# Performance work log

Measured on AMD Instinct MI355X. Metric: run time of the kernel, lower is better.

## Reference

```python
import jax, jax.numpy as jnp
import numpy as np

B, S, E, D = 8, 2048, 1024, 64

def setup_inputs() -> dict:
    key = jax.random.key(0)
    k1, k2, k3, k4 = jax.random.split(key, 4)
    x = jax.random.normal(k1, (B, S, E), dtype=jnp.float32)
    attention_mask = jnp.ones((B, S, S), dtype=jnp.int32)
    scale = 1.0 / np.sqrt(E)
    Wq = jax.random.normal(k2, (E, D), dtype=jnp.float32) * scale
    Wk = jax.random.normal(k3, (E, D), dtype=jnp.float32) * scale
    Wv = jax.random.normal(k4, (E, D), dtype=jnp.float32) * scale
    return {"x": x, "attention_mask": attention_mask, "Wq": Wq, "Wk": Wk, "Wv": Wv}

def reference(x, attention_mask, Wq, Wk, Wv):
    # Q,K,V projections: [B,S,E] @ [E,D] -> [B,S,D]
    Q = jnp.einsum('bse,ed->bsd', x, Wq)
    K = jnp.einsum('bse,ed->bsd', x, Wk)
    V = jnp.einsum('bse,ed->bsd', x, Wv)
    d_head = Q.shape[-1]
    # scores: [B,S,S], scaled by sqrt(dim_head)
    scores = jnp.einsum('bqd,bkd->bqk', Q, K) / jnp.sqrt(jnp.asarray(d_head, Q.dtype))
    scores = jnp.where(attention_mask == 0, jnp.asarray(-jnp.inf, scores.dtype), scores)
    attn = jax.nn.softmax(scores, axis=-1)
    # dropout p=0.0 (eval mode) -> identity
    out = jnp.einsum('bqk,bkd->bqd', attn, V)
    return out
```

## Files before the change

kernel.cpp:

```cpp
#include <hip/hip_runtime.h>
#include <hip/hip_bf16.h>
#include <math.h>


typedef __attribute__((ext_vector_type(8))) short short8;
typedef __attribute__((ext_vector_type(4))) float v4f;

__device__ __forceinline__ unsigned short f2bf(float f) {
  unsigned int u = __float_as_uint(f);
  unsigned int r = (u + 0x7fffu + ((u >> 16) & 1u)) >> 16;
  return (unsigned short)r;
}

__global__ __launch_bounds__(256) void prep_wf(const float* __restrict__ Wq,
                                               const float* __restrict__ Wk,
                                               const float* __restrict__ Wv,
                                               unsigned short* __restrict__ Wf) {
  int t = blockIdx.x * 256 + threadIdx.x;
  int e0 = t * 4;
  int m = e0 >> 16;
  int rem = e0 & 65535;
  int k = rem >> 6, n0 = rem & 63;
  const float* W = (m == 0) ? Wq : (m == 1 ? Wk : Wv);
  float4 f4 = *reinterpret_cast<const float4*>(W + rem);
  int kt = k >> 6, rr = k & 63;
  int kk = rr >> 5, quad = (rr >> 3) & 3, j = k & 7;
  int cbase = kt * 24 + kk;
  float f[4] = {f4.x, f4.y, f4.z, f4.w};
#pragma unroll
  for (int c = 0; c < 4; c++) {
    int N = m * 64 + n0 + c;
    int nt = N >> 4, q = N & 15;
    int o = (((cbase + nt * 2) << 6) | (quad * 16 + q)) * 8 + j;
    Wf[o] = f2bf(f[c]);
  }
}

__global__ __launch_bounds__(512) void proj_kernel(const float* __restrict__ x,
                                                   const unsigned short* __restrict__ Wf,
                                                   unsigned short* __restrict__ Qg,
                                                   unsigned short* __restrict__ Kf,
                                                   unsigned short* __restrict__ Vf) {
  const int tid = threadIdx.x;
  const int w = tid >> 6;
  const int lane = tid & 63;
  const int q = lane & 15, quad = lane >> 4;
  const int rg = w >> 2, ng = w & 3;
  const int m0 = blockIdx.x * 32 + rg * 16;

  const float* xrow = x + (size_t)(m0 + q) * 1024 + quad * 8;
  const unsigned short* Wl = Wf + lane * 8;

  v4f acc[3];
#pragma unroll
  for (int i = 0; i < 3; i++) acc[i] = (v4f)(0.0f);

  float4 acur[4], anext[4];
  auto loadA = [&](int kt, float4 a[4]) {
    const float* p = xrow + kt * 64;
    a[0] = *reinterpret_cast<const float4*>(p);
    a[1] = *reinterpret_cast<const float4*>(p + 4);
    a[2] = *reinterpret_cast<const float4*>(p + 32);
    a[3] = *reinterpret_cast<const float4*>(p + 36);
  };

  short8 bcur[6], bnext[6];
  auto loadB = [&](int kt, short8 bb[6]) {
#pragma unroll
    for (int i = 0; i < 3; i++) {
      const size_t toff = ((size_t)kt * 24 + (ng * 3 + i) * 2) * 512;
      bb[2 * i + 0] = *reinterpret_cast<const short8*>(Wl + toff);
      bb[2 * i + 1] = *reinterpret_cast<const short8*>(Wl + toff + 512);
    }
  };

  loadA(0, acur);
  loadB(0, bcur);

  for (int kt = 0; kt < 16; kt++) {
    if (kt < 15) {
      loadA(kt + 1, anext);
      loadB(kt + 1, bnext);
    }
    short8 af0, af1;
    {
      float* f = reinterpret_cast<float*>(acur);
#pragma unroll
      for (int j = 0; j < 4; j++) { af0[j] = (short)f2bf(f[j]); af0[4 + j] = (short)f2bf(f[4 + j]); }
#pragma unroll
      for (int j = 0; j < 4; j++) { af1[j] = (short)f2bf(f[8 + j]); af1[4 + j] = (short)f2bf(f[12 + j]); }
    }
    __builtin_amdgcn_s_setprio(1);
#pragma unroll
    for (int i = 0; i < 3; i++) {
      acc[i] = __builtin_amdgcn_mfma_f32_16x16x32_bf16(af0, bcur[2 * i + 0], acc[i], 0, 0, 0);
      acc[i] = __builtin_amdgcn_mfma_f32_16x16x32_bf16(af1, bcur[2 * i + 1], acc[i], 0, 0, 0);
    }
    __builtin_amdgcn_s_setprio(0);
#pragma unroll
    for (int i = 0; i < 4; i++) acur[i] = anext[i];
#pragma unroll
    for (int i = 0; i < 6; i++) bcur[i] = bnext[i];
  }

#pragma unroll
  for (int i = 0; i < 3; i++) {
    const int n = (ng * 3 + i) * 16 + q;
#pragma unroll
    for (int r = 0; r < 4; r++) {
      const int m = m0 + quad * 4 + r;
      const unsigned short hv = f2bf(acc[i][r]);
      if (n < 64) {
        Qg[(size_t)m * 64 + n] = hv;
      } else if (n < 128) {
        const int d = n - 64, s = m;
        const int b = s >> 11, srem = s & 2047, g = srem >> 4, qi = srem & 15;
        const int kk2 = d >> 5, quad2 = (d >> 3) & 3, j2 = d & 7;
        Kf[((((size_t)b * 128 + g) * 2 + kk2) * 64 + quad2 * 16 + qi) * 8 + j2] = hv;
      } else {
        const int d = n - 128, s = m;
        const int b = s >> 11, srem = s & 2047, kt2 = srem >> 6, s6 = srem & 63;
        const int kk2 = s6 >> 5, quad2 = (s6 >> 3) & 3, j2 = s6 & 7;
        const int dt = d >> 4, qi = d & 15;
        Vf[(((((size_t)b * 32 + kt2) * 4 + dt) * 2 + kk2) * 64 + quad2 * 16 + qi) * 8 + j2] = hv;
      }
    }
  }
}

__global__ __launch_bounds__(256, 3) void attn_kernel(const unsigned short* __restrict__ Qg,
                                                      const unsigned short* __restrict__ Kf,
                                                      const unsigned short* __restrict__ Vf,
                                                      const int* __restrict__ maskg,
                                                      float* __restrict__ outg) {
  __shared__ __align__(16) unsigned short Pl[4][16][72];

  const int tid = threadIdx.x;
  const int bid = blockIdx.x;
  const int b = bid & 7, qt = bid >> 3;
  const int q0 = qt * 16;
  const int w = tid >> 6, lane = tid & 63;
  const int q = lane & 15, quad = lane >> 4;

  const size_t qbase = ((size_t)b * 2048 + q0 + q) * 64 + quad * 8;
  const short8 qf0 = *reinterpret_cast<const short8*>(&Qg[qbase]);
  const short8 qf1 = *reinterpret_cast<const short8*>(&Qg[qbase + 32]);

  short8 onesf;
#pragma unroll
  for (int j = 0; j < 8; j++) onesf[j] = (short)0x3F80;

  const unsigned short* Kb = Kf + (size_t)b * 131072 + lane * 8;
  const unsigned short* Vb = Vf + (size_t)b * 131072 + lane * 8;
  const int* mb = maskg + ((size_t)b * 2048 + q0 + quad) * 2048 + q * 4;

  v4f o_acc[4], l_acc;
#pragma unroll
  for (int dt = 0; dt < 4; dt++) o_acc[dt] = (v4f)(0.0f);
  l_acc = (v4f)(0.0f);

  const float SC = 0.125f * 1.4426950408889634f;
  const int kt0 = w * 8;

  auto loadK = [&](int kt, short8 kk[8]) {
#pragma unroll
    for (int f = 0; f < 8; f++)
      kk[f] = *reinterpret_cast<const short8*>(Kb + ((size_t)kt * 8 + f) * 512);
  };

  unsigned zb = 0;
  {
    int4 m4[4];
#pragma unroll
    for (int j = 0; j < 4; j++)
      m4[j] = *reinterpret_cast<const int4*>(mb + (size_t)j * 8192 + kt0 * 64);
#pragma unroll
    for (int j = 0; j < 4; j++)
      zb |= ((unsigned)(m4[j].x == 0) << (j * 4)) | ((unsigned)(m4[j].y == 0) << (j * 4 + 1)) |
            ((unsigned)(m4[j].z == 0) << (j * 4 + 2)) | ((unsigned)(m4[j].w == 0) << (j * 4 + 3));
  }

  short8 kcur[8], knext[8];
  loadK(kt0, kcur);

#pragma unroll
  for (int it = 0; it < 8; it++) {
    const int kt = kt0 + it;

    int4 m4[4];
    if (it < 7) {
#pragma unroll
      for (int j = 0; j < 4; j++)
        m4[j] = *reinterpret_cast<const int4*>(mb + (size_t)j * 8192 + (kt + 1) * 64);
    }

    v4f s_acc[4];
    __builtin_amdgcn_s_setprio(1);
#pragma unroll
    for (int nt = 0; nt < 4; nt++) {
      s_acc[nt] = __builtin_amdgcn_mfma_f32_16x16x32_bf16(qf0, kcur[nt * 2 + 0], (v4f)(0.0f), 0, 0, 0);
      s_acc[nt] = __builtin_amdgcn_mfma_f32_16x16x32_bf16(qf1, kcur[nt * 2 + 1], s_acc[nt], 0, 0, 0);
    }
    __builtin_amdgcn_s_setprio(0);

    if (it < 7) loadK(kt + 1, knext);

    short8 vf[8];
#pragma unroll
    for (int f = 0; f < 8; f++)
      vf[f] = *reinterpret_cast<const short8*>(Vb + ((size_t)kt * 8 + f) * 512);

#pragma unroll
    for (int nt = 0; nt < 4; nt++)
#pragma unroll
      for (int r = 0; r < 4; r++)
        Pl[w][quad * 4 + r][nt * 16 + q] = f2bf(exp2f(s_acc[nt][r] * SC));

    if (__any(zb != 0u)) {
#pragma unroll
      for (int j = 0; j < 4; j++)
#pragma unroll
        for (int c = 0; c < 4; c++)
          if ((zb >> (j * 4 + c)) & 1u) Pl[w][j * 4 + quad][q * 4 + c] = 0;
    }

    const short8 pf0 = *reinterpret_cast<const short8*>(&Pl[w][q][quad * 8]);
    const short8 pf1 = *reinterpret_cast<const short8*>(&Pl[w][q][32 + quad * 8]);

    __builtin_amdgcn_s_setprio(1);
#pragma unroll
    for (int dt = 0; dt < 4; dt++) {
      o_acc[dt] = __builtin_amdgcn_mfma_f32_16x16x32_bf16(pf0, vf[dt * 2 + 0], o_acc[dt], 0, 0, 0);
      o_acc[dt] = __builtin_amdgcn_mfma_f32_16x16x32_bf16(pf1, vf[dt * 2 + 1], o_acc[dt], 0, 0, 0);
    }
    l_acc = __builtin_amdgcn_mfma_f32_16x16x32_bf16(pf0, onesf, l_acc, 0, 0, 0);
    l_acc = __builtin_amdgcn_mfma_f32_16x16x32_bf16(pf1, onesf, l_acc, 0, 0, 0);
    __builtin_amdgcn_s_setprio(0);

    if (it < 7) {
#pragma unroll
      for (int f = 0; f < 8; f++) kcur[f] = knext[f];
      zb = 0;
#pragma unroll
      for (int j = 0; j < 4; j++)
        zb |= ((unsigned)(m4[j].x == 0) << (j * 4)) | ((unsigned)(m4[j].y == 0) << (j * 4 + 1)) |
              ((unsigned)(m4[j].z == 0) << (j * 4 + 2)) | ((unsigned)(m4[j].w == 0) << (j * 4 + 3));
    }
  }

  __syncthreads();
  float* Osf = reinterpret_cast<float*>(&Pl[0][0][0]);
  float* Lsf = Osf + 2 * 16 * 68;

  if (w >= 2) {
    const int wi = w - 2;
#pragma unroll
    for (int r = 0; r < 4; r++) {
      const int row = quad * 4 + r;
#pragma unroll
      for (int dt = 0; dt < 4; dt++) Osf[(wi * 16 + row) * 68 + dt * 16 + q] = o_acc[dt][r];
      if (q == 0) Lsf[wi * 16 + row] = l_acc[r];
    }
  }
  __syncthreads();
  if (w < 2) {
#pragma unroll
    for (int r = 0; r < 4; r++) {
      const int row = quad * 4 + r;
#pragma unroll
      for (int dt = 0; dt < 4; dt++) o_acc[dt][r] += Osf[(w * 16 + row) * 68 + dt * 16 + q];
      l_acc[r] += Lsf[w * 16 + row];
    }
  }
  __syncthreads();
  if (w == 1) {
#pragma unroll
    for (int r = 0; r < 4; r++) {
      const int row = quad * 4 + r;
#pragma unroll
      for (int dt = 0; dt < 4; dt++) Osf[row * 68 + dt * 16 + q] = o_acc[dt][r];
      if (q == 0) Lsf[row] = l_acc[r];
    }
  }
  __syncthreads();
  if (w == 0) {
#pragma unroll
    for (int r = 0; r < 4; r++) {
      const int row = quad * 4 + r;
      const float inv = 1.0f / (l_acc[r] + Lsf[row]);
      const size_t orow = ((size_t)b * 2048 + q0 + row) * 64;
#pragma unroll
      for (int dt = 0; dt < 4; dt++)
        outg[orow + dt * 16 + q] = (o_acc[dt][r] + Osf[row * 68 + dt * 16 + q]) * inv;
    }
  }
}

extern "C" void kernel_launch(void* const* d_in, const int* in_sizes, int n_in,
                              void* d_out, int out_size, void* d_ws, size_t ws_size,
                              hipStream_t stream) {
  const float* x = (const float*)d_in[0];
  const int* mask = (const int*)d_in[1];
  const float* Wq = (const float*)d_in[2];
  const float* Wk = (const float*)d_in[3];
  const float* Wv = (const float*)d_in[4];
  float* out = (float*)d_out;

  char* ws = (char*)d_ws;
  unsigned short* Qg = (unsigned short*)(ws);
  unsigned short* Kf = (unsigned short*)(ws + (size_t)(2 << 20));
  unsigned short* Vf = (unsigned short*)(ws + (size_t)(4 << 20));
  unsigned short* Wf = (unsigned short*)(ws + (size_t)(6 << 20));

  prep_wf<<<192, 256, 0, stream>>>(Wq, Wk, Wv, Wf);
  proj_kernel<<<512, 512, 0, stream>>>(x, Wf, Qg, Kf, Vf);
  attn_kernel<<<1024, 256, 0, stream>>>(Qg, Kf, Vf, mask, out);
}
```

Before: 295.0 us.

## Precompute mask bitmasks in prep kernel and drop register double-buffers

Mask reading and compression into 16-bit zero-bitmasks moves from the attention kernel into a widened prep kernel, which also still converts the weights. The attention kernel then reads compact bitmasks instead of int32 mask tiles in its inner loop. Separately, the K and B operand prefetches now write into the current buffers after the MFMAs rather than into separate next buffers, and proj_kernel gets an occupancy hint, all to reduce register pressure. The mask must still be read in full by the prep kernel, and the reused buffers can serialise loads behind compute.

```diff
diff --git a/kernel.cpp b/kernel.cpp
--- a/kernel.cpp
+++ b/kernel.cpp
@@ -12,35 +12,52 @@
   return (unsigned short)r;
 }
 
-__global__ __launch_bounds__(256) void prep_wf(const float* __restrict__ Wq,
-                                               const float* __restrict__ Wk,
-                                               const float* __restrict__ Wv,
-                                               unsigned short* __restrict__ Wf) {
-  int t = blockIdx.x * 256 + threadIdx.x;
-  int e0 = t * 4;
-  int m = e0 >> 16;
-  int rem = e0 & 65535;
-  int k = rem >> 6, n0 = rem & 63;
-  const float* W = (m == 0) ? Wq : (m == 1 ? Wk : Wv);
-  float4 f4 = *reinterpret_cast<const float4*>(W + rem);
-  int kt = k >> 6, rr = k & 63;
-  int kk = rr >> 5, quad = (rr >> 3) & 3, j = k & 7;
-  int cbase = kt * 24 + kk;
-  float f[4] = {f4.x, f4.y, f4.z, f4.w};
-#pragma unroll
-  for (int c = 0; c < 4; c++) {
-    int N = m * 64 + n0 + c;
-    int nt = N >> 4, q = N & 15;
-    int o = (((cbase + nt * 2) << 6) | (quad * 16 + q)) * 8 + j;
-    Wf[o] = f2bf(f[c]);
-  }
-}
-
-__global__ __launch_bounds__(512) void proj_kernel(const float* __restrict__ x,
-                                                   const unsigned short* __restrict__ Wf,
-                                                   unsigned short* __restrict__ Qg,
-                                                   unsigned short* __restrict__ Kf,
-                                                   unsigned short* __restrict__ Vf) {
+__global__ __launch_bounds__(256) void prep_kernel(const float* __restrict__ Wq,
+                                                   const float* __restrict__ Wk,
+                                                   const float* __restrict__ Wv,
+                                                   const int* __restrict__ maskg,
+                                                   unsigned short* __restrict__ Wf,
+                                                   unsigned short* __restrict__ zbg) {
+  const int t = blockIdx.x * 256 + threadIdx.x;
+  const int lane = t & 63, kt = (t >> 6) & 31, qt = (t >> 11) & 127, b = t >> 18;
+  const int q = lane & 15, quad = lane >> 4;
+  const int* mp = maskg + ((size_t)(b * 2048 + qt * 16 + quad)) * 2048 + kt * 64 + q * 4;
+  unsigned zb = 0;
+#pragma unroll
+  for (int j = 0; j < 4; j++) {
+    int4 m4 = *reinterpret_cast<const int4*>(mp + (size_t)j * 8192);
+    zb |= ((unsigned)(m4.x == 0) << (j * 4)) | ((unsigned)(m4.y == 0) << (j * 4 + 1)) |
+          ((unsigned)(m4.z == 0) << (j * 4 + 2)) | ((unsigned)(m4.w == 0) << (j * 4 + 3));
+  }
+  zbg[t] = (unsigned short)zb;
+
+  const bool doW = (t < 49152);
+  if (doW) {
+    int e0 = t * 4;
+    int m = e0 >> 16;
+    int rem = e0 & 65535;
+    int k = rem >> 6, n0 = rem & 63;
+    const float* W = (m == 0) ? Wq : (m == 1 ? Wk : Wv);
+    float4 f4 = *reinterpret_cast<const float4*>(W + rem);
+    int kt2 = k >> 6, rr = k & 63;
+    int kk = rr >> 5, quad2 = (rr >> 3) & 3, j = k & 7;
+    int cbase = kt2 * 24 + kk;
+    float f[4] = {f4.x, f4.y, f4.z, f4.w};
+#pragma unroll
+    for (int c = 0; c < 4; c++) {
+      int N = m * 64 + n0 + c;
+      int nt = N >> 4, qq = N & 15;
+      int o = (((cbase + nt * 2) << 6) | (quad2 * 16 + qq)) * 8 + j;
+      Wf[o] = f2bf(f[c]);
+    }
+  }
+}
+
+__global__ __launch_bounds__(512, 4) void proj_kernel(const float* __restrict__ x,
+                                                      const unsigned short* __restrict__ Wf,
+                                                      unsigned short* __restrict__ Qg,
+                                                      unsigned short* __restrict__ Kf,
+                                                      unsigned short* __restrict__ Vf) {
   const int tid = threadIdx.x;
   const int w = tid >> 6;
   const int lane = tid & 63;
@@ -64,7 +81,7 @@
     a[3] = *reinterpret_cast<const float4*>(p + 36);
   };
 
-  short8 bcur[6], bnext[6];
+  short8 bcur[6];
   auto loadB = [&](int kt, short8 bb[6]) {
 #pragma unroll
     for (int i = 0; i < 3; i++) {
@@ -78,10 +95,7 @@
   loadB(0, bcur);
 
   for (int kt = 0; kt < 16; kt++) {
-    if (kt < 15) {
-      loadA(kt + 1, anext);
-      loadB(kt + 1, bnext);
-    }
+    if (kt < 15) loadA(kt + 1, anext);
     short8 af0, af1;
     {
       float* f = reinterpret_cast<float*>(acur);
@@ -97,10 +111,9 @@
       acc[i] = __builtin_amdgcn_mfma_f32_16x16x32_bf16(af1, bcur[2 * i + 1], acc[i], 0, 0, 0);
     }
     __builtin_amdgcn_s_setprio(0);
+    if (kt < 15) loadB(kt + 1, bcur);
 #pragma unroll
     for (int i = 0; i < 4; i++) acur[i] = anext[i];
-#pragma unroll
-    for (int i = 0; i < 6; i++) bcur[i] = bnext[i];
   }
 
 #pragma unroll
@@ -131,7 +144,7 @@
 __global__ __launch_bounds__(256, 3) void attn_kernel(const unsigned short* __restrict__ Qg,
                                                       const unsigned short* __restrict__ Kf,
                                                       const unsigned short* __restrict__ Vf,
-                                                      const int* __restrict__ maskg,
+                                                      const unsigned short* __restrict__ zbg,
                                                       float* __restrict__ outg) {
   __shared__ __align__(16) unsigned short Pl[4][16][72];
 
@@ -152,7 +165,6 @@
 
   const unsigned short* Kb = Kf + (size_t)b * 131072 + lane * 8;
   const unsigned short* Vb = Vf + (size_t)b * 131072 + lane * 8;
-  const int* mb = maskg + ((size_t)b * 2048 + q0 + quad) * 2048 + q * 4;
 
   v4f o_acc[4], l_acc;
 #pragma unroll
@@ -161,6 +173,13 @@
 
   const float SC = 0.125f * 1.4426950408889634f;
   const int kt0 = w * 8;
+
+  unsigned short zbs[8];
+  {
+    const unsigned short* zbp = zbg + (((size_t)b * 128 + qt) * 32 + kt0) * 64 + lane;
+#pragma unroll
+    for (int it = 0; it < 8; it++) zbs[it] = zbp[it * 64];
+  }
 
   auto loadK = [&](int kt, short8 kk[8]) {
 #pragma unroll
@@ -168,31 +187,12 @@
       kk[f] = *reinterpret_cast<const short8*>(Kb + ((size_t)kt * 8 + f) * 512);
   };
 
-  unsigned zb = 0;
-  {
-    int4 m4[4];
-#pragma unroll
-    for (int j = 0; j < 4; j++)
-      m4[j] = *reinterpret_cast<const int4*>(mb + (size_t)j * 8192 + kt0 * 64);
-#pragma unroll
-    for (int j = 0; j < 4; j++)
-      zb |= ((unsigned)(m4[j].x == 0) << (j * 4)) | ((unsigned)(m4[j].y == 0) << (j * 4 + 1)) |
-            ((unsigned)(m4[j].z == 0) << (j * 4 + 2)) | ((unsigned)(m4[j].w == 0) << (j * 4 + 3));
-  }
-
-  short8 kcur[8], knext[8];
+  short8 kcur[8];
   loadK(kt0, kcur);
 
 #pragma unroll
   for (int it = 0; it < 8; it++) {
     const int kt = kt0 + it;
-
-    int4 m4[4];
-    if (it < 7) {
-#pragma unroll
-      for (int j = 0; j < 4; j++)
-        m4[j] = *reinterpret_cast<const int4*>(mb + (size_t)j * 8192 + (kt + 1) * 64);
-    }
 
     v4f s_acc[4];
     __builtin_amdgcn_s_setprio(1);
@@ -203,7 +203,7 @@
     }
     __builtin_amdgcn_s_setprio(0);
 
-    if (it < 7) loadK(kt + 1, knext);
+    if (it < 7) loadK(kt + 1, kcur);
 
     short8 vf[8];
 #pragma unroll
@@ -216,12 +216,12 @@
       for (int r = 0; r < 4; r++)
         Pl[w][quad * 4 + r][nt * 16 + q] = f2bf(exp2f(s_acc[nt][r] * SC));
 
-    if (__any(zb != 0u)) {
+    if (__any(zbs[it] != 0)) {
 #pragma unroll
       for (int j = 0; j < 4; j++)
 #pragma unroll
         for (int c = 0; c < 4; c++)
-          if ((zb >> (j * 4 + c)) & 1u) Pl[w][j * 4 + quad][q * 4 + c] = 0;
+          if ((zbs[it] >> (j * 4 + c)) & 1u) Pl[w][j * 4 + quad][q * 4 + c] = 0;
     }
 
     const short8 pf0 = *reinterpret_cast<const short8*>(&Pl[w][q][quad * 8]);
@@ -236,16 +236,6 @@
     l_acc = __builtin_amdgcn_mfma_f32_16x16x32_bf16(pf0, onesf, l_acc, 0, 0, 0);
     l_acc = __builtin_amdgcn_mfma_f32_16x16x32_bf16(pf1, onesf, l_acc, 0, 0, 0);
     __builtin_amdgcn_s_setprio(0);
-
-    if (it < 7) {
-#pragma unroll
-      for (int f = 0; f < 8; f++) kcur[f] = knext[f];
-      zb = 0;
-#pragma unroll
-      for (int j = 0; j < 4; j++)
-        zb |= ((unsigned)(m4[j].x == 0) << (j * 4)) | ((unsigned)(m4[j].y == 0) << (j * 4 + 1)) |
-              ((unsigned)(m4[j].z == 0) << (j * 4 + 2)) | ((unsigned)(m4[j].w == 0) << (j * 4 + 3));
-    }
   }
 
   __syncthreads();
@@ -311,8 +301,9 @@
   unsigned short* Kf = (unsigned short*)(ws + (size_t)(2 << 20));
   unsigned short* Vf = (unsigned short*)(ws + (size_t)(4 << 20));
   unsigned short* Wf = (unsigned short*)(ws + (size_t)(6 << 20));
-
-  prep_wf<<<192, 256, 0, stream>>>(Wq, Wk, Wv, Wf);
+  unsigned short* zbg = (unsigned short*)(ws + (size_t)(8 << 20));
+
+  prep_kernel<<<8192, 256, 0, stream>>>(Wq, Wk, Wv, mask, Wf, zbg);
   proj_kernel<<<512, 512, 0, stream>>>(x, Wf, Qg, Kf, Vf);
-  attn_kernel<<<1024, 256, 0, stream>>>(Qg, Kf, Vf, mask, out);
-}
+  attn_kernel<<<1024, 256, 0, stream>>>(Qg, Kf, Vf, zbg, out);
+}
```

Measured after the change: 293.3 us. About the same (-0.6%).
